# Optimization experiments

Measured on AMD Instinct MI355X. Metric: run time of the kernel, lower is better.

## Reference

```python
import jax, jax.numpy as jnp
import numpy as np

B, T, D, H = 8, 4096, 512, 64

def setup_inputs() -> dict:
    key = jax.random.key(0)
    ks = jax.random.split(key, 6)
    s = 0.02  # small init scale so exp(K), exp(wbias) stay numerically tame
    return {
        "x": jax.random.normal(ks[0], (B, T, D), dtype=jnp.float32),
        "wq": jax.random.normal(ks[1], (H, D), dtype=jnp.float32) * s,
        "bq": jnp.zeros((H,), dtype=jnp.float32),
        "wk": jax.random.normal(ks[2], (H, D), dtype=jnp.float32) * s,
        "bk": jnp.zeros((H,), dtype=jnp.float32),
        "wv": jax.random.normal(ks[3], (H, D), dtype=jnp.float32) * s,
        "bv": jnp.zeros((H,), dtype=jnp.float32),
        "wp": jax.random.normal(ks[4], (D, H), dtype=jnp.float32) * s,
        "bp": jnp.zeros((D,), dtype=jnp.float32),
        "wbias": jax.random.normal(ks[5], (T, T), dtype=jnp.float32) * s,
    }

def reference(x, wq, bq, wk, bk, wv, bv, wp, bp, wbias):
    # Q, K, V projections: [B, T, H]
    Q = jnp.einsum('btd,hd->bth', x, wq) + bq
    K = jnp.einsum('btd,hd->bth', x, wk) + bk
    V = jnp.einsum('btd,hd->bth', x, wv) + bv
    ew = jnp.exp(wbias)              # [T, T], computed once
    eK = jnp.exp(K)                  # [B, T, H]
    num = jnp.einsum('ts,bsh->bth', ew, eK * V)
    den = jnp.einsum('ts,bsh->bth', ew, eK)
    Yt = jax.nn.sigmoid(Q) * (num / den)
    # output projection back to dim: [B, T, D]
    return jnp.einsum('bth,dh->btd', Yt, wp) + bp
```

## Files before the change

### kernel.cpp

```cpp
#include <hip/hip_runtime.h>
#include <math.h>

typedef _Float16 f16;
typedef __attribute__((ext_vector_type(8))) _Float16 f16x8;
typedef __attribute__((ext_vector_type(4))) _Float16 f16x4;
typedef __attribute__((ext_vector_type(4))) float f32x4;
typedef __attribute__((ext_vector_type(16))) float f32x16;

#define MFMA16(a, b, c) __builtin_amdgcn_mfma_f32_16x16x32_f16((a), (b), (c), 0, 0, 0)
#define MFMA32(a, b, c) __builtin_amdgcn_mfma_f32_32x32x16_f16((a), (b), (c), 0, 0, 0)

__device__ __forceinline__ void gld16(const f16* g, f16* l) {
  __builtin_amdgcn_global_load_lds(
      (const __attribute__((address_space(1))) unsigned int*)g,
      (__attribute__((address_space(3))) unsigned int*)l, 16, 0, 0);
}

__device__ __forceinline__ f16x8 pack8(const float* src) {
  float4 f0 = *(const float4*)src;
  float4 f1 = *(const float4*)(src + 4);
  f16x8 v;
  v[0] = (f16)f0.x; v[1] = (f16)f0.y; v[2] = (f16)f0.z; v[3] = (f16)f0.w;
  v[4] = (f16)f1.x; v[5] = (f16)f1.y; v[6] = (f16)f1.z; v[7] = (f16)f1.w;
  return v;
}

__global__ __launch_bounds__(256) void k0(const float* __restrict__ x,
                                          const float* __restrict__ wq,
                                          const float* __restrict__ wk,
                                          const float* __restrict__ wv,
                                          const float* __restrict__ wp,
                                          const float* __restrict__ bq,
                                          const float* __restrict__ bk,
                                          const float* __restrict__ bv,
                                          const float* __restrict__ wbias,
                                          f16* __restrict__ ew,
                                          f16* __restrict__ wpf,
                                          f16* __restrict__ sigQ,
                                          f16* __restrict__ XT) {
  __shared__ alignas(16) f16 sW[192 * 64];
  __shared__ alignas(16) f16 sX[64 * 64];
  const int tid = threadIdx.x;

  if (blockIdx.x >= 512) {
    const int pb = blockIdx.x - 512;
    const size_t stride = (size_t)(gridDim.x - 512) * 256;
    const size_t total = (size_t)4096 * 4096 / 4;
    for (size_t i = (size_t)pb * 256 + tid; i < total; i += stride) {
      float4 f = ((const float4*)wbias)[i];
      f16x4 o;
      o.x = (f16)expf(f.x); o.y = (f16)expf(f.y);
      o.z = (f16)expf(f.z); o.w = (f16)expf(f.w);
      ((f16x4*)ew)[i] = o;
    }
    if (pb == 0) {
#pragma unroll
      for (int u = 0; u < 16; ++u) {
        int d = u * 256 + tid;
        int dcb = d >> 8, c = (d >> 6) & 3, l = d & 63;
        const float* src = wp + (size_t)(dcb * 32 + (l & 31)) * 64 + c * 16 + (l >> 5) * 8;
        f16x8 o;
#pragma unroll
        for (int e = 0; e < 8; ++e) o[e] = (f16)src[e];
        *(f16x8*)(wpf + ((size_t)d << 3)) = o;
      }
    }
    return;
  }

  const int wave = tid >> 6, lane = tid & 63;
  const int m0 = blockIdx.x * 64;
  const int l15 = lane & 15;

  f32x4 accQ[4], accK[4], accV[4];
#pragma unroll
  for (int j = 0; j < 4; ++j) {
    accQ[j] = (f32x4){0.f, 0.f, 0.f, 0.f};
    accK[j] = (f32x4){0.f, 0.f, 0.f, 0.f};
    accV[j] = (f32x4){0.f, 0.f, 0.f, 0.f};
  }

  for (int ks = 0; ks < 512; ks += 64) {
#pragma unroll
    for (int u = 0; u < 6; ++u) {
      int un = tid + u * 256;
      int r = un >> 3, c8 = un & 7;
      const float* src = (u < 2) ? (wk + (size_t)r * 512)
                                 : (u < 4) ? (wv + (size_t)(r - 64) * 512)
                                           : (wq + (size_t)(r - 128) * 512);
      *(f16x8*)&sW[r * 64 + ((c8 ^ (r & 7)) * 8)] = pack8(src + ks + c8 * 8);
    }
#pragma unroll
    for (int u = 0; u < 2; ++u) {
      int un = tid + u * 256;
      int r = un >> 3, c8 = un & 7;
      *(f16x8*)&sX[r * 64 + ((c8 ^ (r & 7)) * 8)] =
          pack8(x + (size_t)(m0 + r) * 512 + ks + c8 * 8);
    }
    __syncthreads();
#pragma unroll
    for (int kk = 0; kk < 2; ++kk) {
      const int c = kk * 4 + (lane >> 4);
      const int rK = wave * 16 + l15;
      const int rV = 64 + rK;
      f16x8 aK = *(const f16x8*)&sW[rK * 64 + ((c ^ (rK & 7)) * 8)];
      f16x8 aV = *(const f16x8*)&sW[rV * 64 + ((c ^ (rV & 7)) * 8)];
      f16x8 aQ = *(const f16x8*)&sX[rK * 64 + ((c ^ (rK & 7)) * 8)];
#pragma unroll
      for (int j = 0; j < 4; ++j) {
        const int rX = j * 16 + l15;
        const int rWq = 128 + j * 16 + l15;
        f16x8 bx = *(const f16x8*)&sX[rX * 64 + ((c ^ (rX & 7)) * 8)];
        f16x8 bw = *(const f16x8*)&sW[rWq * 64 + ((c ^ (rWq & 7)) * 8)];
        accK[j] = MFMA16(aK, bx, accK[j]);
        accV[j] = MFMA16(aV, bx, accV[j]);
        accQ[j] = MFMA16(aQ, bw, accQ[j]);
      }
    }
    __syncthreads();
  }
  const int b = m0 >> 12, t0 = m0 & 4095;
#pragma unroll
  for (int j = 0; j < 4; ++j) {
    const int h = j * 16 + l15;
    const float bqv = bq[h];
#pragma unroll
    for (int r = 0; r < 4; ++r) {
      const int m = m0 + wave * 16 + (lane >> 4) * 4 + r;
      const float v = accQ[j][r] + bqv;
      sigQ[(size_t)m * 64 + h] = (f16)(1.f / (1.f + expf(-v)));
    }
  }
#pragma unroll
  for (int r = 0; r < 4; ++r) {
    const int h = wave * 16 + (lane >> 4) * 4 + r;
    const float bkv = bk[h], bvv = bv[h];
    const size_t rowKV = (size_t)(b * 128 + h) * 4096;
    const size_t rowK = (size_t)(b * 128 + 64 + h) * 4096;
#pragma unroll
    for (int j = 0; j < 4; ++j) {
      const int t = t0 + j * 16 + l15;
      const float ek = expf(accK[j][r] + bkv);
      const float ev = accV[j][r] + bvv;
      XT[rowKV + t] = (f16)(ek * ev);
      XT[rowK + t] = (f16)ek;
    }
  }
}

__global__ __launch_bounds__(256) void k2_main(const f16* __restrict__ A,
                                               const f16* __restrict__ Bm,
                                               f16* __restrict__ P) {
  __shared__ alignas(16) f16 smem[2][2][8192];
  const int tid = threadIdx.x;
  const int w = tid >> 6, lane = tid & 63;
  const int wr = w >> 1, wc = w & 1;
  const int bid = blockIdx.x;
  const int x = bid & 7, y = bid >> 3;
  const int mt = x * 4 + (y >> 4);
  const int rem = y & 15;
  const int b = rem >> 1, kh = rem & 1;
  const int m0 = mt * 128;
  const size_t k0 = (size_t)kh * 2048;
  const f16* Ab = A + (size_t)m0 * 4096 + k0;
  const f16* Bb = Bm + (size_t)(b * 128) * 4096 + k0;

  int sRow[4], sCol[4];
#pragma unroll
  for (int u = 0; u < 4; ++u) {
    int d = u * 256 + tid;
    int p = d >> 4, c16 = d & 15;
    int oc = c16 ^ (p & 15);
    sRow[u] = p + 64 * (oc >> 3);
    sCol[u] = (oc & 7) * 8;
  }

  f32x16 accN[2], accD[2];
#pragma unroll
  for (int i = 0; i < 2; ++i)
#pragma unroll
    for (int r = 0; r < 16; ++r) { accN[i][r] = 0.f; accD[i][r] = 0.f; }

#define SB0 __builtin_amdgcn_sched_barrier(0)
#define K2_STAGE(buf, ks)                                                       \
  do {                                                                          \
    _Pragma("unroll") for (int u = 0; u < 4; ++u)                               \
        gld16(Ab + (size_t)sRow[u] * 4096 + (ks) + sCol[u],                     \
              &smem[buf][0][(u * 256 + tid) * 8]);                              \
    _Pragma("unroll") for (int u = 0; u < 4; ++u)                               \
        gld16(Bb + (size_t)sRow[u] * 4096 + (ks) + sCol[u],                     \
              &smem[buf][1][(u * 256 + tid) * 8]);                              \
  } while (0)

  K2_STAGE(0, 0);
  K2_STAGE(1, 64);
  asm volatile("s_waitcnt vmcnt(8)" ::: "memory");
  SB0;
  __builtin_amdgcn_s_barrier();
  SB0;

  const int l31 = lane & 31, l15 = lane & 15, lhi = lane >> 5;
  const int nk = 32;
  for (int t = 0; t < nk; ++t) {
    const int cur = t & 1;
    const f16* pA = smem[cur][0];
    const f16* pB = smem[cur][1];
    __builtin_amdgcn_s_setprio(1);
#pragma unroll
    for (int ks4 = 0; ks4 < 4; ++ks4) {
      const int kcc = ks4 * 2 + lhi;
      f16x8 a0 = *(const f16x8*)&pA[(l31)*128 + (((wr * 8 + kcc) ^ l15) * 8)];
      f16x8 a1 = *(const f16x8*)&pA[(32 + l31) * 128 + (((wr * 8 + kcc) ^ l15) * 8)];
      f16x8 bn = *(const f16x8*)&pB[(wc * 32 + l31) * 128 + ((kcc ^ l15) * 8)];
      f16x8 bd = *(const f16x8*)&pB[(wc * 32 + l31) * 128 + (((8 + kcc) ^ l15) * 8)];
      accN[0] = MFMA32(a0, bn, accN[0]);
      accD[0] = MFMA32(a0, bd, accD[0]);
      accN[1] = MFMA32(a1, bn, accN[1]);
      accD[1] = MFMA32(a1, bd, accD[1]);
    }
    __builtin_amdgcn_s_setprio(0);
    asm volatile("s_waitcnt lgkmcnt(0)" ::: "memory");
    SB0;
    __builtin_amdgcn_s_barrier();
    SB0;
    if (t + 2 < nk) {
      K2_STAGE(cur, (t + 2) * 64);
      asm volatile("s_waitcnt vmcnt(8)" ::: "memory");
    } else {
      asm volatile("s_waitcnt vmcnt(0)" ::: "memory");
    }
    SB0;
    __builtin_amdgcn_s_barrier();
    SB0;
  }
#undef K2_STAGE
#undef SB0

  f16* Pp = P + (size_t)kh * 4194304 + (size_t)(mt * 8 + b) * 16384;
#pragma unroll
  for (int i = 0; i < 2; ++i) {
#pragma unroll
    for (int r = 0; r < 16; ++r) {
      const int crow = wr * 64 + i * 32 + (r & 3) + 8 * (r >> 2) + 4 * lhi;
      Pp[crow * 128 + wc * 32 + l31] = (f16)accN[i][r];
      Pp[crow * 128 + 64 + wc * 32 + l31] = (f16)accD[i][r];
    }
  }
}

__global__ __launch_bounds__(512) void k2_red(const f16* __restrict__ P,
                                              const f16* __restrict__ sigQ,
                                              const f16* __restrict__ wpf,
                                              const float* __restrict__ bp,
                                              float* __restrict__ out) {
  __shared__ alignas(16) f16 sYt[64 * 72];
  const int tid = threadIdx.x;
  const int rid = blockIdx.x;
  const int xcd = rid & 7;
  const int q = rid >> 3;
  const int mt = xcd * 4 + (q & 3);
  const int b = (q >> 2) & 7;
  const int rh = q >> 5;
  const int m0 = mt * 128;
  const f16* P0 = P + (size_t)(mt * 8 + b) * 16384 + rh * 64 * 128;
  const f16* P1 = P0 + 4194304;

  {
    const int row = tid >> 3, c = tid & 7;
    f16x8 n0 = *(const f16x8*)(P0 + row * 128 + c * 8);
    f16x8 n1 = *(const f16x8*)(P1 + row * 128 + c * 8);
    f16x8 d0 = *(const f16x8*)(P0 + row * 128 + 64 + c * 8);
    f16x8 d1 = *(const f16x8*)(P1 + row * 128 + 64 + c * 8);
    f16x8 sq = *(const f16x8*)(sigQ + ((size_t)b * 4096 + m0 + rh * 64 + row) * 64 + c * 8);
    f16x8 yv;
#pragma unroll
    for (int e = 0; e < 8; ++e) {
      const float num = (float)n0[e] + (float)n1[e];
      const float den = (float)d0[e] + (float)d1[e];
      yv[e] = (f16)((float)sq[e] * num / den);
    }
    *(f16x8*)&sYt[row * 72 + c * 8] = yv;
  }
  __syncthreads();

  const int w = tid >> 6, lane = tid & 63;
  const int l31 = lane & 31, lhi = lane >> 5;
  f16x8 ay[2][4];
#pragma unroll
  for (int rg = 0; rg < 2; ++rg)
#pragma unroll
    for (int c = 0; c < 4; ++c)
      ay[rg][c] = *(const f16x8*)&sYt[(rg * 32 + l31) * 72 + c * 16 + lhi * 8];

#pragma unroll
  for (int c2 = 0; c2 < 2; ++c2) {
    const int cbo = w * 2 + c2;
    f32x16 oacc[2];
#pragma unroll
    for (int rg = 0; rg < 2; ++rg)
#pragma unroll
      for (int r = 0; r < 16; ++r) oacc[rg][r] = 0.f;
#pragma unroll
    for (int c = 0; c < 4; ++c) {
      f16x8 bw = *(const f16x8*)(wpf + (((size_t)cbo * 4 + c) * 64 + lane) * 8);
      oacc[0] = MFMA32(ay[0][c], bw, oacc[0]);
      oacc[1] = MFMA32(ay[1][c], bw, oacc[1]);
    }
    const int od = cbo * 32 + l31;
    const float bpv = bp[od];
#pragma unroll
    for (int rg = 0; rg < 2; ++rg) {
#pragma unroll
      for (int r = 0; r < 16; ++r) {
        const int orow = rh * 64 + rg * 32 + (r & 3) + 8 * (r >> 2) + 4 * lhi;
        out[((size_t)(b * 4096 + m0 + orow)) * 512 + od] = oacc[rg][r] + bpv;
      }
    }
  }
}

extern "C" void kernel_launch(void* const* d_in, const int* in_sizes, int n_in,
                              void* d_out, int out_size, void* d_ws, size_t ws_size,
                              hipStream_t stream) {
  const float* x = (const float*)d_in[0];
  const float* wq = (const float*)d_in[1];
  const float* bq = (const float*)d_in[2];
  const float* wk = (const float*)d_in[3];
  const float* bk = (const float*)d_in[4];
  const float* wv = (const float*)d_in[5];
  const float* bv = (const float*)d_in[6];
  const float* wp = (const float*)d_in[7];
  const float* bp = (const float*)d_in[8];
  const float* wbias = (const float*)d_in[9];
  float* out = (float*)d_out;

  char* ws = (char*)d_ws;
  f16* ew = (f16*)(ws);
  f16* XT = (f16*)(ws + 33554432);
  f16* sigQ = (f16*)(ws + 41943040);
  f16* P = (f16*)(ws + 46137344);
  f16* wpf = (f16*)(ws + 62914560);

  k0<<<2560, 256, 0, stream>>>(x, wq, wk, wv, wp, bq, bk, bv, wbias, ew, wpf, sigQ, XT);
  k2_main<<<512, 256, 0, stream>>>(ew, XT, P);
  k2_red<<<512, 512, 0, stream>>>(P, sigQ, wpf, bp, out);
}
```

Measured before the change: 100.4 us.

## Split weight prep into separate kernel and load pre-converted fp16 QKV weights via LDS DMA

Splits the fused prep kernel into two launches. The first does exp(wbias) and converts wq/wk/wv/wp to fp16 once. The second runs the QKV projection and loads the fp16 weight tiles straight into LDS with global_load_lds, with an XOR swizzle on the source column. This removes the fp32-to-fp16 weight conversion that each of the 512 projection blocks used to repeat. The cost is an extra kernel launch, and the projection no longer overlaps with the exp(wbias) work.

```diff
diff --git a/kernel.cpp b/kernel.cpp
--- a/kernel.cpp
+++ b/kernel.cpp
@@ -25,49 +25,54 @@
   return v;
 }
 
-__global__ __launch_bounds__(256) void k0(const float* __restrict__ x,
-                                          const float* __restrict__ wq,
-                                          const float* __restrict__ wk,
-                                          const float* __restrict__ wv,
-                                          const float* __restrict__ wp,
-                                          const float* __restrict__ bq,
-                                          const float* __restrict__ bk,
-                                          const float* __restrict__ bv,
-                                          const float* __restrict__ wbias,
-                                          f16* __restrict__ ew,
-                                          f16* __restrict__ wpf,
-                                          f16* __restrict__ sigQ,
-                                          f16* __restrict__ XT) {
+__global__ __launch_bounds__(256) void prep_ewpw(const float* __restrict__ wb,
+                                                 f16* __restrict__ ew,
+                                                 const float* __restrict__ wq,
+                                                 const float* __restrict__ wk,
+                                                 const float* __restrict__ wv,
+                                                 const float* __restrict__ wp,
+                                                 f16* __restrict__ wqkvb,
+                                                 f16* __restrict__ wpf) {
+  const size_t stride = (size_t)gridDim.x * 256;
+  const size_t total = (size_t)4096 * 4096 / 4;
+  for (size_t i = (size_t)blockIdx.x * 256 + threadIdx.x; i < total; i += stride) {
+    float4 f = ((const float4*)wb)[i];
+    f16x4 o;
+    o.x = (f16)expf(f.x); o.y = (f16)expf(f.y);
+    o.z = (f16)expf(f.z); o.w = (f16)expf(f.w);
+    ((f16x4*)ew)[i] = o;
+  }
+  if (blockIdx.x < 128) {
+    int i = blockIdx.x * 256 + threadIdx.x;
+    wqkvb[i] = (f16)wk[i];
+    wqkvb[32768 + i] = (f16)wv[i];
+    wqkvb[65536 + i] = (f16)wq[i];
+  }
+  if (blockIdx.x == 128) {
+    const int tid = threadIdx.x;
+#pragma unroll
+    for (int u = 0; u < 16; ++u) {
+      int d = u * 256 + tid;
+      int dcb = d >> 8, c = (d >> 6) & 3, l = d & 63;
+      const float* src = wp + (size_t)(dcb * 32 + (l & 31)) * 64 + c * 16 + (l >> 5) * 8;
+      f16x8 o;
+#pragma unroll
+      for (int e = 0; e < 8; ++e) o[e] = (f16)src[e];
+      *(f16x8*)(wpf + ((size_t)d << 3)) = o;
+    }
+  }
+}
+
+__global__ __launch_bounds__(256) void k1_qkv(const float* __restrict__ x,
+                                              const f16* __restrict__ wqkvb,
+                                              const float* __restrict__ bq,
+                                              const float* __restrict__ bk,
+                                              const float* __restrict__ bv,
+                                              f16* __restrict__ sigQ,
+                                              f16* __restrict__ XT) {
   __shared__ alignas(16) f16 sW[192 * 64];
   __shared__ alignas(16) f16 sX[64 * 64];
   const int tid = threadIdx.x;
-
-  if (blockIdx.x >= 512) {
-    const int pb = blockIdx.x - 512;
-    const size_t stride = (size_t)(gridDim.x - 512) * 256;
-    const size_t total = (size_t)4096 * 4096 / 4;
-    for (size_t i = (size_t)pb * 256 + tid; i < total; i += stride) {
-      float4 f = ((const float4*)wbias)[i];
-      f16x4 o;
-      o.x = (f16)expf(f.x); o.y = (f16)expf(f.y);
-      o.z = (f16)expf(f.z); o.w = (f16)expf(f.w);
-      ((f16x4*)ew)[i] = o;
-    }
-    if (pb == 0) {
-#pragma unroll
-      for (int u = 0; u < 16; ++u) {
-        int d = u * 256 + tid;
-        int dcb = d >> 8, c = (d >> 6) & 3, l = d & 63;
-        const float* src = wp + (size_t)(dcb * 32 + (l & 31)) * 64 + c * 16 + (l >> 5) * 8;
-        f16x8 o;
-#pragma unroll
-        for (int e = 0; e < 8; ++e) o[e] = (f16)src[e];
-        *(f16x8*)(wpf + ((size_t)d << 3)) = o;
-      }
-    }
-    return;
-  }
-
   const int wave = tid >> 6, lane = tid & 63;
   const int m0 = blockIdx.x * 64;
   const int l15 = lane & 15;
@@ -80,15 +85,15 @@
     accV[j] = (f32x4){0.f, 0.f, 0.f, 0.f};
   }
 
+  const int sc8 = tid & 7;
+  const int wr8 = (tid >> 3) & 7;
+  const int wcol = (sc8 ^ wr8) * 8;
+
   for (int ks = 0; ks < 512; ks += 64) {
 #pragma unroll
-    for (int u = 0; u < 6; ++u) {
-      int un = tid + u * 256;
-      int r = un >> 3, c8 = un & 7;
-      const float* src = (u < 2) ? (wk + (size_t)r * 512)
-                                 : (u < 4) ? (wv + (size_t)(r - 64) * 512)
-                                           : (wq + (size_t)(r - 128) * 512);
-      *(f16x8*)&sW[r * 64 + ((c8 ^ (r & 7)) * 8)] = pack8(src + ks + c8 * 8);
+    for (int q = 0; q < 6; ++q) {
+      int r = q * 32 + (tid >> 3);
+      gld16(wqkvb + (size_t)r * 512 + ks + wcol, &sW[r * 64 + sc8 * 8]);
     }
 #pragma unroll
     for (int u = 0; u < 2; ++u) {
@@ -339,9 +344,11 @@
   f16* XT = (f16*)(ws + 33554432);
   f16* sigQ = (f16*)(ws + 41943040);
   f16* P = (f16*)(ws + 46137344);
-  f16* wpf = (f16*)(ws + 62914560);
-
-  k0<<<2560, 256, 0, stream>>>(x, wq, wk, wv, wp, bq, bk, bv, wbias, ew, wpf, sigQ, XT);
+  f16* wqkvb = (f16*)(ws + 62914560);
+  f16* wpf = (f16*)(ws + 63111168);
+
+  prep_ewpw<<<4096, 256, 0, stream>>>(wbias, ew, wq, wk, wv, wp, wqkvb, wpf);
+  k1_qkv<<<512, 256, 0, stream>>>(x, wqkvb, bq, bk, bv, sigQ, XT);
   k2_main<<<512, 256, 0, stream>>>(ew, XT, P);
   k2_red<<<512, 512, 0, stream>>>(P, sigQ, wpf, bp, out);
 }
```

New measurement: 96.18 us. -4.2%, faster.
